# Kernel tuning notes

Hardware: AMD Instinct MI355X
Metric: run time of the kernel (lower is better)

The kernel has to match this reference:

```python
import math
import jax, jax.numpy as jnp
import numpy as np

S, B, H, D = 2048, 1, 16, 128  # seq, batch, heads, head_dim (hard-coded in source)
COEFF = 1.0  # layer_num = 1
NORM_FACTOR = math.sqrt(2048 / 16) * COEFF  # sqrt(HIDDEN/NUM_HEADS) * coeff


def setup_inputs() -> dict:
    key = jax.random.key(0)
    k1, k2, k3, k4, k5 = jax.random.split(key, 5)
    query_layer = jax.random.normal(k1, (S, B, H, D), dtype=jnp.float32)
    key_layer = jax.random.normal(k2, (S, B, H, D), dtype=jnp.float32)
    value_layer = jax.random.normal(k3, (S, B, H, D), dtype=jnp.float32)
    # causal mask, True = masked (Megatron convention)
    attention_mask = jnp.triu(jnp.ones((S, S), dtype=bool), k=1)[None, None]
    # per-head SVD right-singular-vector matrices (orthonormal-ish; random here)
    svd_qk = jax.random.normal(k4, (H, D, D), dtype=jnp.float32) / math.sqrt(D)
    svd_v = jax.random.normal(k5, (H, D, D), dtype=jnp.float32) / math.sqrt(D)
    return {"query_layer": query_layer, "key_layer": key_layer,
            "value_layer": value_layer, "attention_mask": attention_mask,
            "svd_qk": svd_qk, "svd_v": svd_v}


def reference(query_layer, key_layer, value_layer, attention_mask, svd_qk, svd_v):
    # q/k/v: [S, 1, H, D] -> project each head through its SVD matrix
    q = jnp.einsum('shd,hde->hse', query_layer[:, 0], svd_qk)  # [H,S,D]
    k = jnp.einsum('shd,hde->hse', key_layer[:, 0], svd_qk)    # [H,S,D]
    # qk_drop = 0 -> h_mask zeroing of columns is a no-op (faithfully skipped)
    scores = jnp.einsum('hqe,hke->hqk', q, k) / NORM_FACTOR    # [H,S,S]
    mask = attention_mask[0, 0]                                 # [S,S] bool
    scores = jnp.where(mask, jnp.float32(-10000.0), scores)
    # FusedScaleMaskSoftmax: scale by coeff, re-mask, softmax
    scaled = jnp.where(mask, jnp.float32(-10000.0), scores * COEFF)
    probs = jax.nn.softmax(scaled, axis=-1)                     # [H,S,S]
    # attention dropout is identity in eval mode
    v = jnp.einsum('shd,hde->hse', value_layer[:, 0], svd_v)    # [H,S,D]
    # vlinear_drop = 0 -> column zeroing is a no-op
    ctx = jnp.einsum('hqk,hke->qhe', probs, v)                  # [S,H,D]
    return ctx.reshape(S, B, H * D)                             # [S,1,2048]
```

## Files before the change

kernel.cpp:

```cpp
#include <hip/hip_runtime.h>
#include <hip/hip_bf16.h>
#include <math.h>

#define S_LEN 2048
#define NHEAD 16
#define DHEAD 128

typedef __attribute__((ext_vector_type(8)))  _Float16 f16x8;
typedef __attribute__((ext_vector_type(4)))  _Float16 f16x4;
typedef __attribute__((ext_vector_type(4)))  float    f32x4;
typedef __attribute__((ext_vector_type(16))) float    f32x16;

__device__ __forceinline__ void permswap(unsigned &a, unsigned &b) {
    asm volatile("v_permlane32_swap_b32 %0, %1" : "+v"(a), "+v"(b));
}

typedef __attribute__((address_space(3))) unsigned int lds_u32;
typedef __attribute__((address_space(1))) const unsigned int glb_u32;
__device__ __forceinline__ void gload16(const void* g, void* l) {
    __builtin_amdgcn_global_load_lds((glb_u32*)g, (lds_u32*)l, 16, 0, 0);
}

__global__ __launch_bounds__(256) void transpose_w_kernel(
    const float* __restrict__ w_qk, const float* __restrict__ w_v,
    _Float16* __restrict__ wqk_t, _Float16* __restrict__ wv_t)
{
    __shared__ float tile[32][33];
    const int mat = blockIdx.z;
    const int h   = blockIdx.y;
    const int t0  = blockIdx.x;
    const int dt  = (t0 >> 2) * 32;
    const int et  = (t0 & 3) * 32;
    const float* src = (mat ? w_v : w_qk) + (size_t)h * DHEAD * DHEAD;
    _Float16*   dst = (mat ? wv_t : wqk_t) + (size_t)h * DHEAD * DHEAD;
    const int tx = threadIdx.x & 31, ty = threadIdx.x >> 5;
#pragma unroll
    for (int k = 0; k < 4; ++k)
        tile[ty + 8 * k][tx] = src[(size_t)(dt + ty + 8 * k) * DHEAD + et + tx];
    __syncthreads();
#pragma unroll
    for (int k = 0; k < 4; ++k)
        dst[(size_t)(et + ty + 8 * k) * DHEAD + dt + tx] = (_Float16)tile[tx][ty + 8 * k];
}

__global__ __launch_bounds__(512, 4) void proj_kernel(
    const float* __restrict__ q_in, const float* __restrict__ k_in,
    const float* __restrict__ v_in,
    const _Float16* __restrict__ wqk_t, const _Float16* __restrict__ wv_t,
    _Float16* __restrict__ Qp, _Float16* __restrict__ Kp, _Float16* __restrict__ Vt)
{
    __shared__ _Float16 xs[3][64][136];

    const int h   = blockIdx.x & 15;
    const int rb  = blockIdx.x >> 4;
    const int tid = threadIdx.x;

#pragma unroll
    for (int m = 0; m < 3; ++m) {
        const float* xin = (m == 0) ? q_in : (m == 1) ? k_in : v_in;
#pragma unroll
        for (int k = 0; k < 4; ++k) {
            const int v   = tid + k * 512;
            const int row = v >> 5;
            const int c4  = v & 31;
            const f32x4 x = *(const f32x4*)(xin +
                ((size_t)(rb * 64 + row) * NHEAD + h) * DHEAD + c4 * 4);
            f16x4 xh;
#pragma unroll
            for (int i = 0; i < 4; ++i) xh[i] = (_Float16)x[i];
            *(f16x4*)&xs[m][row][c4 * 4] = xh;
        }
    }
    __syncthreads();

    const int w    = tid >> 6;
    const int lane = tid & 63;
    const int r16  = lane & 15;
    const int kg   = lane >> 4;
    const int rw   = w & 3;
    const int ch   = w >> 2;
    const int s_base = rb * 64 + rw * 16;
    const float INV_NORM = 0.12752211758f;

    f16x8 aq[4], ak[4], av[4];
#pragma unroll
    for (int kb = 0; kb < 4; ++kb) {
        const int d0 = kb * 32 + kg * 8;
        aq[kb] = *(const f16x8*)&xs[0][rw * 16 + r16][d0];
        ak[kb] = *(const f16x8*)&xs[1][rw * 16 + r16][d0];
        av[kb] = *(const f16x8*)&xs[2][rw * 16 + r16][d0];
    }

    const _Float16* wq_h = wqk_t + (size_t)h * DHEAD * DHEAD;
    const _Float16* wv_h = wv_t  + (size_t)h * DHEAD * DHEAD;

#pragma unroll 2
    for (int cc = 0; cc < 4; ++cc) {
        const int cb = ch * 4 + cc;
        f32x4 accq = {0.f, 0.f, 0.f, 0.f};
        f32x4 acck = {0.f, 0.f, 0.f, 0.f};
        f32x4 accv = {0.f, 0.f, 0.f, 0.f};
        const int c = cb * 16 + r16;
#pragma unroll
        for (int kb = 0; kb < 4; ++kb) {
            const f16x8 bqk = *(const f16x8*)(wq_h + (size_t)c * DHEAD + kb * 32 + kg * 8);
            const f16x8 bv  = *(const f16x8*)(wv_h + (size_t)c * DHEAD + kb * 32 + kg * 8);
            accq = __builtin_amdgcn_mfma_f32_16x16x32_f16(bqk, aq[kb], accq, 0, 0, 0);
            acck = __builtin_amdgcn_mfma_f32_16x16x32_f16(bqk, ak[kb], acck, 0, 0, 0);
            accv = __builtin_amdgcn_mfma_f32_16x16x32_f16(av[kb], bv,  accv, 0, 0, 0);
        }
        f16x4 qv, kv4;
#pragma unroll
        for (int jj = 0; jj < 4; ++jj) {
            qv[jj]  = (_Float16)(accq[jj] * INV_NORM);
            kv4[jj] = (_Float16)acck[jj];
        }
        *(f16x4*)(Qp + ((size_t)h * S_LEN + s_base + r16) * DHEAD + cb * 16 + kg * 4) = qv;
        *(f16x4*)(Kp + ((size_t)h * S_LEN + s_base + r16) * DHEAD + cb * 16 + kg * 4) = kv4;
        f16x4 vvv;
#pragma unroll
        for (int jj = 0; jj < 4; ++jj) vvv[jj] = (_Float16)accv[jj];
        *(f16x4*)(Vt + ((size_t)h * DHEAD + c) * S_LEN + s_base + kg * 4) = vvv;
    }
}

__device__ __forceinline__ void stage_k4(const _Float16* kbase, char* kst,
                                         int w, int lane, int par, int inext,
                                         int jmax_lock) {
#pragma unroll
    for (int cidx = 0; cidx < 4; ++cidx) {
        const int c    = 4 * w + cidx;
        const int slot = c >> 3;
        const int cc   = c & 7;
        const int jn   = 4 * inext + slot;
        if (jn < jmax_lock) {
            const int A    = cc * 1024 + lane * 16;
            const int srcO = A ^ (((A >> 8) & 15) << 4);
            const char* g  = (const char*)kbase + (size_t)jn * 8192 + srcO;
            char*       l  = kst + (size_t)(slot * 2 + par) * 8192
                                 + cc * 1024;
            gload16(g, l);
        }
    }
}

__global__ __launch_bounds__(512, 2) void attn_kernel(
    const _Float16* __restrict__ Qp, const _Float16* __restrict__ Kp,
    const _Float16* __restrict__ Vt, float* __restrict__ out)
{
    __shared__ _Float16 Kst[8][4096];
    __shared__ _Float16 obuf[2][3][32][132];
    __shared__ float    mlbuf[2][3][2][32];

    const int id  = blockIdx.x + (blockIdx.y << 4);
    const int xb  = id >> 4;
    const int h   = (id & 7) + 8 * ((id >> 3) & 1);

    const int w    = threadIdx.x >> 6;
    const int lane = threadIdx.x & 63;
    const int q    = lane & 31;
    const int hi   = lane >> 5;

    const int role = w & 3;
    const int qsub = w >> 2;

    const _Float16* kbase = Kp + (size_t)h * S_LEN * DHEAD;
    const _Float16* vbase = Vt + (size_t)h * DHEAD * S_LEN;

    const int lqk = q * DHEAD + hi * 8;
    const int lv  = q * S_LEN + hi * 8;
    const int swq = (q & 15) << 4;

    for (int ph = 0; ph < 2; ++ph) {
        const int t     = ph ? xb : (31 - xb);
        const int q0w   = t * 64 + qsub * 32;
        const int jmax  = 2 * t + 1 + qsub;
        const int jlock = 2 * t + 2;
        const int I     = (jlock + 3) >> 2;
        const int q_abs = q0w + q;

        const _Float16* qbase = Qp + ((size_t)h * S_LEN + q0w) * DHEAD;
        f16x8 qf[8];
#pragma unroll
        for (int m = 0; m < 8; ++m)
            qf[m] = *(const f16x8*)(qbase + lqk + m * 16);

        f32x16 acc[4];
#pragma unroll
        for (int e = 0; e < 4; ++e)
#pragma unroll
            for (int i = 0; i < 16; ++i) acc[e][i] = 0.f;
        float m_run = -1e30f, l_run = 0.f;

        stage_k4(kbase, (char*)Kst, w, lane, 0, 0, jlock);

        int p = 0;
        for (int it = 0; it < I; ++it, p ^= 1) {
            __syncthreads();

            const int j   = 4 * it + role;
            const bool act = (j < jmax);
            const int kv0 = j * 32;

            f16x8 vf[8];
            if (act) {
#pragma unroll
                for (int e = 0; e < 4; ++e) {
                    const _Float16* vp = vbase + (size_t)e * 32 * S_LEN + lv + kv0;
                    vf[2 * e]     = *(const f16x8*)(vp);
                    vf[2 * e + 1] = *(const f16x8*)(vp + 16);
                }
            }

            f16x8 kf[8];
            if (act) {
                const char* kt = (const char*)&Kst[role * 2 + p][0];
#pragma unroll
                for (int m = 0; m < 8; ++m) {
                    const int L = q * 256 + m * 32 + hi * 16;
                    kf[m] = *(const f16x8*)(kt + (L ^ swq));
                }
            }

            if (it + 1 < I)
                stage_k4(kbase, (char*)Kst, w, lane, p ^ 1, it + 1, jlock);

            if (act) {
                f32x16 s0, s1;
#pragma unroll
                for (int i = 0; i < 16; ++i) { s0[i] = 0.f; s1[i] = 0.f; }
                __builtin_amdgcn_s_setprio(1);
#pragma unroll
                for (int m = 0; m < 8; m += 2) {
                    s0 = __builtin_amdgcn_mfma_f32_32x32x16_f16(kf[m],     qf[m],     s0, 0, 0, 0);
                    s1 = __builtin_amdgcn_mfma_f32_32x32x16_f16(kf[m + 1], qf[m + 1], s1, 0, 0, 0);
                }
                __builtin_amdgcn_s_setprio(0);

                f32x16 sv = s0 + s1;

                if (kv0 == q0w) {
#pragma unroll
                    for (int i = 0; i < 16; ++i) {
                        const int krel = (i & 3) + 8 * (i >> 2) + 4 * hi;
                        if (kv0 + krel > q_abs) sv[i] = -1e30f;
                    }
                }

                float t0 = fmaxf(sv[0], sv[1]),  t1 = fmaxf(sv[2], sv[3]);
                float t2 = fmaxf(sv[4], sv[5]),  t3 = fmaxf(sv[6], sv[7]);
                float t4 = fmaxf(sv[8], sv[9]),  t5 = fmaxf(sv[10], sv[11]);
                float t6 = fmaxf(sv[12], sv[13]), t7 = fmaxf(sv[14], sv[15]);
                t0 = fmaxf(t0, t1); t2 = fmaxf(t2, t3);
                t4 = fmaxf(t4, t5); t6 = fmaxf(t6, t7);
                float tm = fmaxf(fmaxf(t0, t2), fmaxf(t4, t6));
                tm = fmaxf(tm, __shfl_xor(tm, 32, 64));

                if (!__all(tm - m_run <= 8.0f)) {
                    const float mnew = fmaxf(m_run, tm);
                    const float corr = exp2f(m_run - mnew);
                    l_run *= corr;
#pragma unroll
                    for (int e = 0; e < 4; ++e)
#pragma unroll
                        for (int i = 0; i < 16; ++i) acc[e][i] *= corr;
                    m_run = mnew;
                }

#pragma unroll
                for (int i = 0; i < 16; ++i) sv[i] = exp2f(sv[i] - m_run);
                float r0 = (sv[0] + sv[1]) + (sv[2] + sv[3]);
                float r1 = (sv[4] + sv[5]) + (sv[6] + sv[7]);
                float r2 = (sv[8] + sv[9]) + (sv[10] + sv[11]);
                float r3 = (sv[12] + sv[13]) + (sv[14] + sv[15]);
                float rs = (r0 + r1) + (r2 + r3);

                unsigned u0 = __builtin_bit_cast(unsigned, __builtin_amdgcn_cvt_pkrtz(sv[0],  sv[1]));
                unsigned u1 = __builtin_bit_cast(unsigned, __builtin_amdgcn_cvt_pkrtz(sv[2],  sv[3]));
                unsigned u2 = __builtin_bit_cast(unsigned, __builtin_amdgcn_cvt_pkrtz(sv[4],  sv[5]));
                unsigned u3 = __builtin_bit_cast(unsigned, __builtin_amdgcn_cvt_pkrtz(sv[6],  sv[7]));
                unsigned u4 = __builtin_bit_cast(unsigned, __builtin_amdgcn_cvt_pkrtz(sv[8],  sv[9]));
                unsigned u5 = __builtin_bit_cast(unsigned, __builtin_amdgcn_cvt_pkrtz(sv[10], sv[11]));
                unsigned u6 = __builtin_bit_cast(unsigned, __builtin_amdgcn_cvt_pkrtz(sv[12], sv[13]));
                unsigned u7 = __builtin_bit_cast(unsigned, __builtin_amdgcn_cvt_pkrtz(sv[14], sv[15]));
                permswap(u0, u2); permswap(u1, u3);
                permswap(u4, u6); permswap(u5, u7);
                union uf8 { unsigned w[4]; f16x8 v; };
                uf8 p0; p0.w[0] = u0; p0.w[1] = u1; p0.w[2] = u2; p0.w[3] = u3;
                uf8 p1; p1.w[0] = u4; p1.w[1] = u5; p1.w[2] = u6; p1.w[3] = u7;

                __builtin_amdgcn_s_setprio(1);
#pragma unroll
                for (int e = 0; e < 4; ++e) {
                    acc[e] = __builtin_amdgcn_mfma_f32_32x32x16_f16(vf[2 * e],     p0.v, acc[e], 0, 0, 0);
                    acc[e] = __builtin_amdgcn_mfma_f32_32x32x16_f16(vf[2 * e + 1], p1.v, acc[e], 0, 0, 0);
                }
                __builtin_amdgcn_s_setprio(0);

                rs += __shfl_xor(rs, 32, 64);
                l_run += rs;
            }
        }

        if (role != 0) {
            if (hi == 0) {
                mlbuf[qsub][role - 1][0][q] = m_run;
                mlbuf[qsub][role - 1][1][q] = l_run;
            }
#pragma unroll
            for (int e = 0; e < 4; ++e)
#pragma unroll
                for (int i = 0; i < 16; ++i) {
                    const int erow = e * 32 + (i & 3) + 8 * (i >> 2) + 4 * hi;
                    obuf[qsub][role - 1][q][erow] = (_Float16)acc[e][i];
                }
        }
        __syncthreads();
        if (role == 0) {
            const float m1 = mlbuf[qsub][0][0][q], l1 = mlbuf[qsub][0][1][q];
            const float m2 = mlbuf[qsub][1][0][q], l2 = mlbuf[qsub][1][1][q];
            const float m3 = mlbuf[qsub][2][0][q], l3 = mlbuf[qsub][2][1][q];
            const float ms = fmaxf(fmaxf(m_run, m1), fmaxf(m2, m3));
            const float c0 = exp2f(m_run - ms);
            const float c1 = exp2f(m1 - ms);
            const float c2 = exp2f(m2 - ms);
            const float c3 = exp2f(m3 - ms);
            const float rinv = 1.0f / (l_run * c0 + l1 * c1 + l2 * c2 + l3 * c3);
            float* orow = out + (size_t)q_abs * (NHEAD * DHEAD) + h * DHEAD;
#pragma unroll
            for (int e = 0; e < 4; ++e) {
#pragma unroll
                for (int g = 0; g < 4; ++g) {
                    f32x4 vv;
#pragma unroll
                    for (int c = 0; c < 4; ++c) {
                        const int i = g * 4 + c;
                        const int erow = e * 32 + 8 * g + 4 * hi + c;
                        vv[c] = (acc[e][i] * c0
                                 + (float)obuf[qsub][0][q][erow] * c1
                                 + (float)obuf[qsub][1][q][erow] * c2
                                 + (float)obuf[qsub][2][q][erow] * c3) * rinv;
                    }
                    *(f32x4*)(orow + e * 32 + 8 * g + 4 * hi) = vv;
                }
            }
        }
        __syncthreads();
    }
}

extern "C" void kernel_launch(void* const* d_in, const int* in_sizes, int n_in,
                              void* d_out, int out_size, void* d_ws, size_t ws_size,
                              hipStream_t stream) {
    const float* q_in = (const float*)d_in[0];
    const float* k_in = (const float*)d_in[1];
    const float* v_in = (const float*)d_in[2];
    const float* w_qk = (const float*)d_in[4];
    const float* w_v  = (const float*)d_in[5];
    float* out = (float*)d_out;

    const size_t mat_elems = (size_t)NHEAD * S_LEN * DHEAD;
    const size_t w_elems   = (size_t)NHEAD * DHEAD * DHEAD;
    _Float16* Qp   = (_Float16*)d_ws;
    _Float16* Kp   = Qp + mat_elems;
    _Float16* Vt   = Kp + mat_elems;
    _Float16* Wqkt = Vt + mat_elems;
    _Float16* Wvt  = Wqkt + w_elems;

    transpose_w_kernel<<<dim3(16, NHEAD, 2), dim3(256), 0, stream>>>(w_qk, w_v, Wqkt, Wvt);
    proj_kernel<<<dim3(NHEAD * 32), dim3(512), 0, stream>>>(q_in, k_in, v_in, Wqkt, Wvt, Qp, Kp, Vt);
    attn_kernel<<<dim3(16, NHEAD), dim3(512), 0, stream>>>(Qp, Kp, Vt, out);
}
```

Measured before the change: 87.07 us.

## Load K tiles directly from global memory instead of LDS double-buffered staging

Removes the shared-memory double-buffered K staging (global_load_lds with swizzle) and the per-iteration block-wide barrier. Each wave now reads its K tile straight from global memory into registers, like V, and loops only over its own active key blocks. This drops the synchronisation and the idle-wave iterations and frees 64KB of LDS, which could help occupancy. In exchange, K is no longer shared across the two q-subgroup waves, so global/L2 traffic rises and load latency is no longer hidden by prefetch.

```diff
diff --git a/kernel.cpp b/kernel.cpp
--- a/kernel.cpp
+++ b/kernel.cpp
@@ -13,12 +13,6 @@
 
 __device__ __forceinline__ void permswap(unsigned &a, unsigned &b) {
     asm volatile("v_permlane32_swap_b32 %0, %1" : "+v"(a), "+v"(b));
-}
-
-typedef __attribute__((address_space(3))) unsigned int lds_u32;
-typedef __attribute__((address_space(1))) const unsigned int glb_u32;
-__device__ __forceinline__ void gload16(const void* g, void* l) {
-    __builtin_amdgcn_global_load_lds((glb_u32*)g, (lds_u32*)l, 16, 0, 0);
 }
 
 __global__ __launch_bounds__(256) void transpose_w_kernel(
@@ -124,31 +118,10 @@
     }
 }
 
-__device__ __forceinline__ void stage_k4(const _Float16* kbase, char* kst,
-                                         int w, int lane, int par, int inext,
-                                         int jmax_lock) {
-#pragma unroll
-    for (int cidx = 0; cidx < 4; ++cidx) {
-        const int c    = 4 * w + cidx;
-        const int slot = c >> 3;
-        const int cc   = c & 7;
-        const int jn   = 4 * inext + slot;
-        if (jn < jmax_lock) {
-            const int A    = cc * 1024 + lane * 16;
-            const int srcO = A ^ (((A >> 8) & 15) << 4);
-            const char* g  = (const char*)kbase + (size_t)jn * 8192 + srcO;
-            char*       l  = kst + (size_t)(slot * 2 + par) * 8192
-                                 + cc * 1024;
-            gload16(g, l);
-        }
-    }
-}
-
 __global__ __launch_bounds__(512, 2) void attn_kernel(
     const _Float16* __restrict__ Qp, const _Float16* __restrict__ Kp,
     const _Float16* __restrict__ Vt, float* __restrict__ out)
 {
-    __shared__ _Float16 Kst[8][4096];
     __shared__ _Float16 obuf[2][3][32][132];
     __shared__ float    mlbuf[2][3][2][32];
 
@@ -169,14 +142,11 @@
 
     const int lqk = q * DHEAD + hi * 8;
     const int lv  = q * S_LEN + hi * 8;
-    const int swq = (q & 15) << 4;
 
     for (int ph = 0; ph < 2; ++ph) {
         const int t     = ph ? xb : (31 - xb);
         const int q0w   = t * 64 + qsub * 32;
         const int jmax  = 2 * t + 1 + qsub;
-        const int jlock = 2 * t + 2;
-        const int I     = (jlock + 3) >> 2;
         const int q_abs = q0w + q;
 
         const _Float16* qbase = Qp + ((size_t)h * S_LEN + q0w) * DHEAD;
@@ -192,114 +162,96 @@
             for (int i = 0; i < 16; ++i) acc[e][i] = 0.f;
         float m_run = -1e30f, l_run = 0.f;
 
-        stage_k4(kbase, (char*)Kst, w, lane, 0, 0, jlock);
-
-        int p = 0;
-        for (int it = 0; it < I; ++it, p ^= 1) {
-            __syncthreads();
-
-            const int j   = 4 * it + role;
-            const bool act = (j < jmax);
+        for (int j = role; j < jmax; j += 4) {
             const int kv0 = j * 32;
 
+            const _Float16* kp = kbase + (size_t)kv0 * DHEAD + lqk;
+            f16x8 kf[8];
+#pragma unroll
+            for (int m = 0; m < 8; ++m)
+                kf[m] = *(const f16x8*)(kp + m * 16);
+
             f16x8 vf[8];
-            if (act) {
-#pragma unroll
-                for (int e = 0; e < 4; ++e) {
-                    const _Float16* vp = vbase + (size_t)e * 32 * S_LEN + lv + kv0;
-                    vf[2 * e]     = *(const f16x8*)(vp);
-                    vf[2 * e + 1] = *(const f16x8*)(vp + 16);
+#pragma unroll
+            for (int e = 0; e < 4; ++e) {
+                const _Float16* vp = vbase + (size_t)e * 32 * S_LEN + lv + kv0;
+                vf[2 * e]     = *(const f16x8*)(vp);
+                vf[2 * e + 1] = *(const f16x8*)(vp + 16);
+            }
+
+            f32x16 s0, s1;
+#pragma unroll
+            for (int i = 0; i < 16; ++i) { s0[i] = 0.f; s1[i] = 0.f; }
+            __builtin_amdgcn_s_setprio(1);
+#pragma unroll
+            for (int m = 0; m < 8; m += 2) {
+                s0 = __builtin_amdgcn_mfma_f32_32x32x16_f16(kf[m],     qf[m],     s0, 0, 0, 0);
+                s1 = __builtin_amdgcn_mfma_f32_32x32x16_f16(kf[m + 1], qf[m + 1], s1, 0, 0, 0);
+            }
+            __builtin_amdgcn_s_setprio(0);
+
+            f32x16 sv = s0 + s1;
+
+            if (kv0 == q0w) {
+#pragma unroll
+                for (int i = 0; i < 16; ++i) {
+                    const int krel = (i & 3) + 8 * (i >> 2) + 4 * hi;
+                    if (kv0 + krel > q_abs) sv[i] = -1e30f;
                 }
             }
 
-            f16x8 kf[8];
-            if (act) {
-                const char* kt = (const char*)&Kst[role * 2 + p][0];
-#pragma unroll
-                for (int m = 0; m < 8; ++m) {
-                    const int L = q * 256 + m * 32 + hi * 16;
-                    kf[m] = *(const f16x8*)(kt + (L ^ swq));
-                }
-            }
-
-            if (it + 1 < I)
-                stage_k4(kbase, (char*)Kst, w, lane, p ^ 1, it + 1, jlock);
-
-            if (act) {
-                f32x16 s0, s1;
-#pragma unroll
-                for (int i = 0; i < 16; ++i) { s0[i] = 0.f; s1[i] = 0.f; }
-                __builtin_amdgcn_s_setprio(1);
-#pragma unroll
-                for (int m = 0; m < 8; m += 2) {
-                    s0 = __builtin_amdgcn_mfma_f32_32x32x16_f16(kf[m],     qf[m],     s0, 0, 0, 0);
-                    s1 = __builtin_amdgcn_mfma_f32_32x32x16_f16(kf[m + 1], qf[m + 1], s1, 0, 0, 0);
-                }
-                __builtin_amdgcn_s_setprio(0);
-
-                f32x16 sv = s0 + s1;
-
-                if (kv0 == q0w) {
-#pragma unroll
-                    for (int i = 0; i < 16; ++i) {
-                        const int krel = (i & 3) + 8 * (i >> 2) + 4 * hi;
-                        if (kv0 + krel > q_abs) sv[i] = -1e30f;
-                    }
-                }
-
-                float t0 = fmaxf(sv[0], sv[1]),  t1 = fmaxf(sv[2], sv[3]);
-                float t2 = fmaxf(sv[4], sv[5]),  t3 = fmaxf(sv[6], sv[7]);
-                float t4 = fmaxf(sv[8], sv[9]),  t5 = fmaxf(sv[10], sv[11]);
-                float t6 = fmaxf(sv[12], sv[13]), t7 = fmaxf(sv[14], sv[15]);
-                t0 = fmaxf(t0, t1); t2 = fmaxf(t2, t3);
-                t4 = fmaxf(t4, t5); t6 = fmaxf(t6, t7);
-                float tm = fmaxf(fmaxf(t0, t2), fmaxf(t4, t6));
-                tm = fmaxf(tm, __shfl_xor(tm, 32, 64));
-
-                if (!__all(tm - m_run <= 8.0f)) {
-                    const float mnew = fmaxf(m_run, tm);
-                    const float corr = exp2f(m_run - mnew);
-                    l_run *= corr;
-#pragma unroll
-                    for (int e = 0; e < 4; ++e)
-#pragma unroll
-                        for (int i = 0; i < 16; ++i) acc[e][i] *= corr;
-                    m_run = mnew;
-                }
-
-#pragma unroll
-                for (int i = 0; i < 16; ++i) sv[i] = exp2f(sv[i] - m_run);
-                float r0 = (sv[0] + sv[1]) + (sv[2] + sv[3]);
-                float r1 = (sv[4] + sv[5]) + (sv[6] + sv[7]);
-                float r2 = (sv[8] + sv[9]) + (sv[10] + sv[11]);
-                float r3 = (sv[12] + sv[13]) + (sv[14] + sv[15]);
-                float rs = (r0 + r1) + (r2 + r3);
-
-                unsigned u0 = __builtin_bit_cast(unsigned, __builtin_amdgcn_cvt_pkrtz(sv[0],  sv[1]));
-                unsigned u1 = __builtin_bit_cast(unsigned, __builtin_amdgcn_cvt_pkrtz(sv[2],  sv[3]));
-                unsigned u2 = __builtin_bit_cast(unsigned, __builtin_amdgcn_cvt_pkrtz(sv[4],  sv[5]));
-                unsigned u3 = __builtin_bit_cast(unsigned, __builtin_amdgcn_cvt_pkrtz(sv[6],  sv[7]));
-                unsigned u4 = __builtin_bit_cast(unsigned, __builtin_amdgcn_cvt_pkrtz(sv[8],  sv[9]));
-                unsigned u5 = __builtin_bit_cast(unsigned, __builtin_amdgcn_cvt_pkrtz(sv[10], sv[11]));
-                unsigned u6 = __builtin_bit_cast(unsigned, __builtin_amdgcn_cvt_pkrtz(sv[12], sv[13]));
-                unsigned u7 = __builtin_bit_cast(unsigned, __builtin_amdgcn_cvt_pkrtz(sv[14], sv[15]));
-                permswap(u0, u2); permswap(u1, u3);
-                permswap(u4, u6); permswap(u5, u7);
-                union uf8 { unsigned w[4]; f16x8 v; };
-                uf8 p0; p0.w[0] = u0; p0.w[1] = u1; p0.w[2] = u2; p0.w[3] = u3;
-                uf8 p1; p1.w[0] = u4; p1.w[1] = u5; p1.w[2] = u6; p1.w[3] = u7;
-
-                __builtin_amdgcn_s_setprio(1);
-#pragma unroll
-                for (int e = 0; e < 4; ++e) {
-                    acc[e] = __builtin_amdgcn_mfma_f32_32x32x16_f16(vf[2 * e],     p0.v, acc[e], 0, 0, 0);
-                    acc[e] = __builtin_amdgcn_mfma_f32_32x32x16_f16(vf[2 * e + 1], p1.v, acc[e], 0, 0, 0);
-                }
-                __builtin_amdgcn_s_setprio(0);
-
-                rs += __shfl_xor(rs, 32, 64);
-                l_run += rs;
-            }
+            float t0 = fmaxf(sv[0], sv[1]),  t1 = fmaxf(sv[2], sv[3]);
+            float t2 = fmaxf(sv[4], sv[5]),  t3 = fmaxf(sv[6], sv[7]);
+            float t4 = fmaxf(sv[8], sv[9]),  t5 = fmaxf(sv[10], sv[11]);
+            float t6 = fmaxf(sv[12], sv[13]), t7 = fmaxf(sv[14], sv[15]);
+            t0 = fmaxf(t0, t1); t2 = fmaxf(t2, t3);
+            t4 = fmaxf(t4, t5); t6 = fmaxf(t6, t7);
+            float tm = fmaxf(fmaxf(t0, t2), fmaxf(t4, t6));
+            tm = fmaxf(tm, __shfl_xor(tm, 32, 64));
+
+            if (!__all(tm - m_run <= 8.0f)) {
+                const float mnew = fmaxf(m_run, tm);
+                const float corr = exp2f(m_run - mnew);
+                l_run *= corr;
+#pragma unroll
+                for (int e = 0; e < 4; ++e)
+#pragma unroll
+                    for (int i = 0; i < 16; ++i) acc[e][i] *= corr;
+                m_run = mnew;
+            }
+
+#pragma unroll
+            for (int i = 0; i < 16; ++i) sv[i] = exp2f(sv[i] - m_run);
+            float r0 = (sv[0] + sv[1]) + (sv[2] + sv[3]);
+            float r1 = (sv[4] + sv[5]) + (sv[6] + sv[7]);
+            float r2 = (sv[8] + sv[9]) + (sv[10] + sv[11]);
+            float r3 = (sv[12] + sv[13]) + (sv[14] + sv[15]);
+            float rs = (r0 + r1) + (r2 + r3);
+
+            unsigned u0 = __builtin_bit_cast(unsigned, __builtin_amdgcn_cvt_pkrtz(sv[0],  sv[1]));
+            unsigned u1 = __builtin_bit_cast(unsigned, __builtin_amdgcn_cvt_pkrtz(sv[2],  sv[3]));
+            unsigned u2 = __builtin_bit_cast(unsigned, __builtin_amdgcn_cvt_pkrtz(sv[4],  sv[5]));
+            unsigned u3 = __builtin_bit_cast(unsigned, __builtin_amdgcn_cvt_pkrtz(sv[6],  sv[7]));
+            unsigned u4 = __builtin_bit_cast(unsigned, __builtin_amdgcn_cvt_pkrtz(sv[8],  sv[9]));
+            unsigned u5 = __builtin_bit_cast(unsigned, __builtin_amdgcn_cvt_pkrtz(sv[10], sv[11]));
+            unsigned u6 = __builtin_bit_cast(unsigned, __builtin_amdgcn_cvt_pkrtz(sv[12], sv[13]));
+            unsigned u7 = __builtin_bit_cast(unsigned, __builtin_amdgcn_cvt_pkrtz(sv[14], sv[15]));
+            permswap(u0, u2); permswap(u1, u3);
+            permswap(u4, u6); permswap(u5, u7);
+            union uf8 { unsigned w[4]; f16x8 v; };
+            uf8 p0; p0.w[0] = u0; p0.w[1] = u1; p0.w[2] = u2; p0.w[3] = u3;
+            uf8 p1; p1.w[0] = u4; p1.w[1] = u5; p1.w[2] = u6; p1.w[3] = u7;
+
+            __builtin_amdgcn_s_setprio(1);
+#pragma unroll
+            for (int e = 0; e < 4; ++e) {
+                acc[e] = __builtin_amdgcn_mfma_f32_32x32x16_f16(vf[2 * e],     p0.v, acc[e], 0, 0, 0);
+                acc[e] = __builtin_amdgcn_mfma_f32_32x32x16_f16(vf[2 * e + 1], p1.v, acc[e], 0, 0, 0);
+            }
+            __builtin_amdgcn_s_setprio(0);
+
+            rs += __shfl_xor(rs, 32, 64);
+            l_run += rs;
         }
 
         if (role != 0) {
```

After: 103.9 us. +19.4%, slower.
